# Kernel optimization log

Hardware: AMD Instinct MI355X
Metric: run time of the kernel (lower is better)

The kernel has to match this reference:

```python
import jax, jax.numpy as jnp
import numpy as np

DIM = 256
HEADS = 8
WINDOWS = (1, 2, 4)
B, H, W = 1, 64, 64


def _integral(a):
    # double cumsum over last two dims, then zero-pad one row/col at top/left
    s = jnp.cumsum(jnp.cumsum(a, axis=-2), axis=-1)
    pad = [(0, 0)] * (a.ndim - 2) + [(1, 0), (1, 0)]
    return jnp.pad(s, pad)


def _box(P, ws, Ho, Wo):
    # replicate-pad then box-difference; equivalent to the 2x2 [[1,-1],[-1,1]]
    # kernel conv2d with dilation=ws applied in the torch module.
    tp = ws - 1
    r = tp // 2
    l = tp - r
    pad = [(0, 0)] * (P.ndim - 2) + [(l, r), (l, r)]
    Pp = jnp.pad(P, pad, mode='edge')
    return (Pp[..., ws:ws + Ho, ws:ws + Wo] - Pp[..., ws:ws + Ho, :Wo]
            - Pp[..., :Ho, ws:ws + Wo] + Pp[..., :Ho, :Wo])


def setup_inputs() -> dict:
    key = jax.random.key(0)
    ks = jax.random.split(key, 6)
    x = jax.random.normal(ks[0], (B, DIM, H, W), jnp.float32)
    Wq = jax.random.normal(ks[1], (DIM, DIM), jnp.float32) * 0.05
    Wk = jax.random.normal(ks[2], (DIM, DIM), jnp.float32) * 0.05
    Wv = jax.random.normal(ks[3], (DIM, DIM), jnp.float32) * 0.05
    Wout = jax.random.normal(ks[4], (DIM, DIM * len(WINDOWS)), jnp.float32) * 0.05
    bout = jnp.zeros((DIM,), jnp.float32)
    return {"x": x, "Wq": Wq, "Wk": Wk, "Wv": Wv, "Wout": Wout, "bout": bout}


def reference(x, Wq, Wk, Wv, Wout, bout):
    b, C, Hh, Ww = x.shape
    h = HEADS
    d = C // h
    # 1x1 convs (no bias)
    q = jnp.einsum('bchw,oc->bohw', x, Wq).reshape(b * h, d, Hh, Ww)
    k = jnp.einsum('bchw,oc->bohw', x, Wk).reshape(b * h, d, Hh, Ww)
    v = jnp.einsum('bchw,oc->bohw', x, Wv).reshape(b * h, d, Hh, Ww)
    q = jax.nn.sigmoid(q)
    k = jax.nn.sigmoid(k)
    v = v / jnp.maximum(jnp.linalg.norm(v, axis=1, keepdims=True), 1e-12)

    Ik = _integral(k)                                  # (bh, d, H+1, W+1)
    Ikv = _integral(jnp.einsum('bfhw,bghw->bfghw', k, v))  # (bh, d, d, H+1, W+1)

    outs = []
    for w in WINDOWS:
        ws = Hh // w
        wk = _box(Ik, ws, Hh, Ww)    # (bh, d, H, W)
        wkv = _box(Ikv, ws, Hh, Ww)  # (bh, d, d, H, W)
        attn = jnp.einsum('bdhw,bdfhw->bfhw', q, wkv)
        norm = jnp.einsum('bdhw,bdhw->bhw', q, wk)
        attn = attn / (norm[:, None] + 1e-6)
        outs.append(attn.reshape(b, C, Hh, Ww))
    o = jnp.concatenate(outs, axis=1)  # (b, C*len(WINDOWS), H, W)
    return jnp.einsum('bchw,oc->bohw', o, Wout) + bout[None, :, None, None]
```

## Files before the change

kernel.cpp:

```cpp
#include <hip/hip_runtime.h>
#include <math.h>

#define NPIX 4096
#define CHSZ 3145728
#define NRMSZ 98304

template <int CTRL, int RM>
__device__ __forceinline__ float dpp_add(float x) {
    int xi = __builtin_bit_cast(int, x);
    int sh = __builtin_amdgcn_update_dpp(0, xi, CTRL, RM, 0xf, false);
    return x + __builtin_bit_cast(float, sh);
}

__device__ __forceinline__ float wave_iscan(float x) {
    x = dpp_add<0x111, 0xf>(x);
    x = dpp_add<0x112, 0xf>(x);
    x = dpp_add<0x114, 0xf>(x);
    x = dpp_add<0x118, 0xf>(x);
    x = dpp_add<0x142, 0xa>(x);
    x = dpp_add<0x143, 0xc>(x);
    return x;
}

__device__ __forceinline__ void lds_barrier() {
    asm volatile("s_waitcnt lgkmcnt(0)" ::: "memory");
    __builtin_amdgcn_s_barrier();
    __builtin_amdgcn_sched_barrier(0);
}

__global__ __launch_bounds__(256) void qkv_kernel(
    const float* __restrict__ x, const float* __restrict__ Wq,
    const float* __restrict__ Wk, const float* __restrict__ Wv,
    float* __restrict__ qo, float* __restrict__ ko, float* __restrict__ vo)
{
    const int pt = blockIdx.x * 128;
    const int ot = blockIdx.y * 32;
    const int mat = blockIdx.z;
    const float* __restrict__ W = (mat == 0) ? Wq : ((mat == 1) ? Wk : Wv);
    float* __restrict__ out = (mat == 0) ? qo : ((mat == 1) ? ko : vo);

    __shared__ __align__(16) float Xs[32][132];
    __shared__ __align__(16) float Wt[32][36];

    const int t = threadIdx.x;
    const int pc = t & 31;
    const int oc = t >> 5;
    const int xc = t >> 5;
    const int xp = (t & 31) << 2;
    const int lo = t >> 3;
    const int lg = (t & 7) << 2;

    float4 xf[4];
    float4 wf;
#pragma unroll
    for (int i = 0; i < 4; i++)
        xf[i] = *reinterpret_cast<const float4*>(x + (xc + 8 * i) * NPIX + pt + xp);
    wf = *reinterpret_cast<const float4*>(W + (ot + lo) * 256 + lg);

    float acc[4][4];
#pragma unroll
    for (int j = 0; j < 4; j++)
#pragma unroll
        for (int i = 0; i < 4; i++) acc[j][i] = 0.f;

    for (int kt = 0; kt < 256; kt += 32) {
#pragma unroll
        for (int i = 0; i < 4; i++)
            *reinterpret_cast<float4*>(&Xs[xc + 8 * i][xp]) = xf[i];
        Wt[lg + 0][lo] = wf.x;
        Wt[lg + 1][lo] = wf.y;
        Wt[lg + 2][lo] = wf.z;
        Wt[lg + 3][lo] = wf.w;
        __syncthreads();
        if (kt + 32 < 256) {
#pragma unroll
            for (int i = 0; i < 4; i++)
                xf[i] = *reinterpret_cast<const float4*>(
                    x + (kt + 32 + xc + 8 * i) * NPIX + pt + xp);
            wf = *reinterpret_cast<const float4*>(W + (ot + lo) * 256 + kt + 32 + lg);
        }
#pragma unroll
        for (int kk = 0; kk < 32; kk++) {
            float4 a = *reinterpret_cast<const float4*>(&Xs[kk][pc << 2]);
            float av[4] = {a.x, a.y, a.z, a.w};
            float4 b4 = *reinterpret_cast<const float4*>(&Wt[kk][oc << 2]);
            float bv[4] = {b4.x, b4.y, b4.z, b4.w};
#pragma unroll
            for (int j = 0; j < 4; j++)
#pragma unroll
                for (int i = 0; i < 4; i++)
                    acc[j][i] = fmaf(bv[j], av[i], acc[j][i]);
        }
        __syncthreads();
    }

    if (mat < 2) {
#pragma unroll
        for (int j = 0; j < 4; j++) {
            const int o = ot + (oc << 2) + j;
            float4 r;
            r.x = 1.f / (1.f + __expf(-acc[j][0]));
            r.y = 1.f / (1.f + __expf(-acc[j][1]));
            r.z = 1.f / (1.f + __expf(-acc[j][2]));
            r.w = 1.f / (1.f + __expf(-acc[j][3]));
            *reinterpret_cast<float4*>(out + o * NPIX + pt + (pc << 2)) = r;
        }
    } else {
        float* scratch = &Xs[0][0];
        __syncthreads();
#pragma unroll
        for (int i = 0; i < 4; i++) {
            float ss = 0.f;
#pragma unroll
            for (int j = 0; j < 4; j++) ss += acc[j][i] * acc[j][i];
            scratch[oc * 128 + (pc << 2) + i] = ss;
        }
        __syncthreads();
        float scale[4];
#pragma unroll
        for (int i = 0; i < 4; i++) {
            float tot = 0.f;
#pragma unroll
            for (int g = 0; g < 8; g++) tot += scratch[g * 128 + (pc << 2) + i];
            scale[i] = 1.f / fmaxf(sqrtf(tot), 1e-12f);
        }
#pragma unroll
        for (int j = 0; j < 4; j++) {
            const int o = ot + (oc << 2) + j;
            float4 r;
            r.x = acc[j][0] * scale[0];
            r.y = acc[j][1] * scale[1];
            r.z = acc[j][2] * scale[2];
            r.w = acc[j][3] * scale[3];
            *reinterpret_cast<float4*>(out + o * NPIX + pt + (pc << 2)) = r;
        }
    }
}

template <int PD>
__global__ __launch_bounds__(512) void attn_kernel(
    const float* __restrict__ q, const float* __restrict__ k,
    const float* __restrict__ v, float* __restrict__ num, float* __restrict__ nrm)
{
    const int f = blockIdx.x;
    const int head = blockIdx.y;
    const int dg = blockIdx.z;
    const bool isnorm = (f == 32);

    const float* __restrict__ kh = k + (head * 32 + dg * PD) * NPIX;
    const float* __restrict__ qh = q + (head * 32 + dg * PD) * NPIX;
    const float* __restrict__ vf = v + (head * 32 + (isnorm ? 0 : f)) * NPIX;

    __shared__ __align__(16) float Pt[2][65][68];
    __shared__ float csum[2][8][68];

    const int t = threadIdx.x;
    const int lane = t & 63;
    const int wv = t >> 6;

    for (int i = t; i < 2 * 65 * 68; i += 512) (&Pt[0][0][0])[i] = 0.f;

    float vreg[8], kcur[8];
#pragma unroll
    for (int i = 0; i < 8; i++) {
        const int r = wv * 8 + i;
        vreg[i] = isnorm ? 1.f : vf[r * 64 + lane];
        kcur[i] = kh[r * 64 + lane];
    }

    float acc[3][8];
#pragma unroll
    for (int w = 0; w < 3; w++)
#pragma unroll
        for (int i = 0; i < 8; i++) acc[w][i] = 0.f;

    float pv[8], runcur;
    {
        float run = 0.f;
#pragma unroll
        for (int i = 0; i < 8; i++) {
            float rs = wave_iscan(kcur[i] * vreg[i]);
            pv[i] = run;
            run += rs;
        }
        csum[0][wv][lane] = run;
        runcur = run;
        if (PD > 1) {
#pragma unroll
            for (int i = 0; i < 8; i++)
                kcur[i] = kh[1 * NPIX + (wv * 8 + i) * 64 + lane];
        }
    }
    lds_barrier();

    float pvn[8], runn;
    for (int dd = 0; dd < PD; dd++) {
        const int b = dd & 1;
        float off = 0.f;
#pragma unroll
        for (int w2 = 0; w2 < 7; w2++) if (w2 < wv) off += csum[b][w2][lane];
#pragma unroll
        for (int s = 0; s < 2; s++) {
            float4 r4 = make_float4(pv[4 * s] + off, pv[4 * s + 1] + off,
                                    pv[4 * s + 2] + off, pv[4 * s + 3] + off);
            *reinterpret_cast<float4*>(&Pt[b][lane + 1][wv * 8 + 4 * s]) = r4;
        }
        if (wv == 7) Pt[b][lane + 1][64] = off + runcur;
        float qv[8];
#pragma unroll
        for (int g = 0; g < 2; g++)
#pragma unroll
            for (int j = 0; j < 4; j++)
                qv[g * 4 + j] = qh[dd * NPIX + ((wv + 8 * g) * 4 + j) * 64 + lane];
        if (dd + 1 < PD) {
            float run = 0.f;
#pragma unroll
            for (int i = 0; i < 8; i++) {
                float rs = wave_iscan(kcur[i] * vreg[i]);
                pvn[i] = run;
                run += rs;
            }
            csum[b ^ 1][wv][lane] = run;
            runn = run;
            if (dd + 2 < PD) {
#pragma unroll
                for (int i = 0; i < 8; i++)
                    kcur[i] = kh[(dd + 2) * NPIX + (wv * 8 + i) * 64 + lane];
            }
        }
        lds_barrier();
#pragma unroll
        for (int g = 0; g < 2; g++) {
            const int y0 = (wv + 8 * g) * 4;
#pragma unroll
            for (int w = 0; w < 3; w++) {
                const int hw = 32 >> w;
                const int xlo = max(lane - hw, 0);
                const int xhi = min(lane + hw, 64);
                float c0, c1, c2, c3;
                if (y0 + 3 <= hw) {
                    float4 A4 = *reinterpret_cast<const float4*>(&Pt[b][xhi][y0 + hw]);
                    float4 B4 = *reinterpret_cast<const float4*>(&Pt[b][xlo][y0 + hw]);
                    c0 = A4.x - B4.x; c1 = A4.y - B4.y;
                    c2 = A4.z - B4.z; c3 = A4.w - B4.w;
                } else if (y0 + hw >= 64) {
                    float As = Pt[b][xhi][64];
                    float Bs = Pt[b][xlo][64];
                    float4 C4 = *reinterpret_cast<const float4*>(&Pt[b][xhi][y0 - hw]);
                    float4 E4 = *reinterpret_cast<const float4*>(&Pt[b][xlo][y0 - hw]);
                    const float ab = As - Bs;
                    c0 = ab - (C4.x - E4.x); c1 = ab - (C4.y - E4.y);
                    c2 = ab - (C4.z - E4.z); c3 = ab - (C4.w - E4.w);
                } else {
                    float4 A4 = *reinterpret_cast<const float4*>(&Pt[b][xhi][y0 + hw]);
                    float4 B4 = *reinterpret_cast<const float4*>(&Pt[b][xlo][y0 + hw]);
                    float4 C4 = *reinterpret_cast<const float4*>(&Pt[b][xhi][y0 - hw]);
                    float4 E4 = *reinterpret_cast<const float4*>(&Pt[b][xlo][y0 - hw]);
                    c0 = (A4.x - B4.x) - (C4.x - E4.x);
                    c1 = (A4.y - B4.y) - (C4.y - E4.y);
                    c2 = (A4.z - B4.z) - (C4.z - E4.z);
                    c3 = (A4.w - B4.w) - (C4.w - E4.w);
                }
                acc[w][g * 4 + 0] = fmaf(qv[g * 4 + 0], c0, acc[w][g * 4 + 0]);
                acc[w][g * 4 + 1] = fmaf(qv[g * 4 + 1], c1, acc[w][g * 4 + 1]);
                acc[w][g * 4 + 2] = fmaf(qv[g * 4 + 2], c2, acc[w][g * 4 + 2]);
                acc[w][g * 4 + 3] = fmaf(qv[g * 4 + 3], c3, acc[w][g * 4 + 3]);
            }
        }
        if (dd + 1 < PD) {
#pragma unroll
            for (int i = 0; i < 8; i++) pv[i] = pvn[i];
            runcur = runn;
        }
    }

    float* __restrict__ nout = num + (size_t)dg * CHSZ;
    float* __restrict__ rout = nrm + (size_t)dg * NRMSZ;
#pragma unroll
    for (int w = 0; w < 3; w++) {
#pragma unroll
        for (int g = 0; g < 2; g++) {
#pragma unroll
            for (int j = 0; j < 4; j++) {
                const int px = ((wv + 8 * g) * 4 + j) * 64 + lane;
                const float val = acc[w][g * 4 + j];
                if (isnorm) rout[(w * 8 + head) * NPIX + px] = val;
                else        nout[((w * 8 + head) * 32 + f) * NPIX + px] = val;
            }
        }
    }
}

template <int NS>
__global__ __launch_bounds__(256) void out_kernel(
    const float* __restrict__ num, const float* __restrict__ nrm,
    const float* __restrict__ Wout, float* __restrict__ obuf)
{
    const int pt = blockIdx.x * 64;
    const int ot = blockIdx.y * 64;
    const int kt0 = blockIdx.z * 12;
    __shared__ __align__(16) float As[32][68];
    __shared__ __align__(16) float Wt[32][68];
    const int t = threadIdx.x;
    const int pc = t & 15;
    const int oc = t >> 4;
    const int xc = t >> 4;
    const int xp = (t & 15) << 2;
    const int lo = t & 63;
    const int lc = (t >> 6) << 2;

    float4 nv[NS][2], mv[NS], wf[2];
#pragma unroll
    for (int s = 0; s < NS; s++) {
#pragma unroll
        for (int i = 0; i < 2; i++)
            nv[s][i] = *reinterpret_cast<const float4*>(
                num + (size_t)s * CHSZ + (size_t)(kt0 * 32 + xc + 16 * i) * NPIX + pt + xp);
        mv[s] = *reinterpret_cast<const float4*>(
            nrm + (size_t)s * NRMSZ + kt0 * NPIX + pt + xp);
    }
    wf[0] = *reinterpret_cast<const float4*>(Wout + (ot + lo) * 768 + kt0 * 32 + lc);
    wf[1] = *reinterpret_cast<const float4*>(Wout + (ot + lo) * 768 + kt0 * 32 + lc + 16);

    float acc[4][4];
#pragma unroll
    for (int j = 0; j < 4; j++)
#pragma unroll
        for (int i = 0; i < 4; i++) acc[j][i] = 0.f;

    for (int kt = kt0; kt < kt0 + 12; kt++) {
        float4 ms = mv[0];
#pragma unroll
        for (int s = 1; s < NS; s++) {
            ms.x += mv[s].x; ms.y += mv[s].y; ms.z += mv[s].z; ms.w += mv[s].w;
        }
        float4 rv;
        rv.x = 1.f / (ms.x + 1e-6f); rv.y = 1.f / (ms.y + 1e-6f);
        rv.z = 1.f / (ms.z + 1e-6f); rv.w = 1.f / (ms.w + 1e-6f);
#pragma unroll
        for (int i = 0; i < 2; i++) {
            float4 r = nv[0][i];
#pragma unroll
            for (int s = 1; s < NS; s++) {
                r.x += nv[s][i].x; r.y += nv[s][i].y;
                r.z += nv[s][i].z; r.w += nv[s][i].w;
            }
            r.x *= rv.x; r.y *= rv.y; r.z *= rv.z; r.w *= rv.w;
            *reinterpret_cast<float4*>(&As[xc + 16 * i][xp]) = r;
        }
#pragma unroll
        for (int i = 0; i < 2; i++) {
            Wt[lc + 16 * i + 0][lo] = wf[i].x;
            Wt[lc + 16 * i + 1][lo] = wf[i].y;
            Wt[lc + 16 * i + 2][lo] = wf[i].z;
            Wt[lc + 16 * i + 3][lo] = wf[i].w;
        }
        __syncthreads();
        if (kt + 1 < kt0 + 12) {
#pragma unroll
            for (int s = 0; s < NS; s++) {
#pragma unroll
                for (int i = 0; i < 2; i++)
                    nv[s][i] = *reinterpret_cast<const float4*>(
                        num + (size_t)s * CHSZ +
                        (size_t)((kt + 1) * 32 + xc + 16 * i) * NPIX + pt + xp);
                mv[s] = *reinterpret_cast<const float4*>(
                    nrm + (size_t)s * NRMSZ + (kt + 1) * NPIX + pt + xp);
            }
            wf[0] = *reinterpret_cast<const float4*>(
                Wout + (ot + lo) * 768 + (kt + 1) * 32 + lc);
            wf[1] = *reinterpret_cast<const float4*>(
                Wout + (ot + lo) * 768 + (kt + 1) * 32 + lc + 16);
        }
#pragma unroll
        for (int kk = 0; kk < 32; kk++) {
            float4 a = *reinterpret_cast<const float4*>(&As[kk][pc << 2]);
            float av[4] = {a.x, a.y, a.z, a.w};
            float4 b4 = *reinterpret_cast<const float4*>(&Wt[kk][oc << 2]);
            float bv[4] = {b4.x, b4.y, b4.z, b4.w};
#pragma unroll
            for (int j = 0; j < 4; j++)
#pragma unroll
                for (int i = 0; i < 4; i++)
                    acc[j][i] = fmaf(bv[j], av[i], acc[j][i]);
        }
        __syncthreads();
    }

    float* __restrict__ ob = obuf + (size_t)blockIdx.z * 1048576;
#pragma unroll
    for (int j = 0; j < 4; j++) {
        const int o = ot + (oc << 2) + j;
        float4 r;
        r.x = acc[j][0]; r.y = acc[j][1]; r.z = acc[j][2]; r.w = acc[j][3];
        *reinterpret_cast<float4*>(ob + o * NPIX + pt + (pc << 2)) = r;
    }
}

__global__ __launch_bounds__(256) void kmerge_kernel(
    const float* __restrict__ obuf, const float* __restrict__ bout,
    float* __restrict__ out)
{
    const int i4 = (blockIdx.x * 256 + threadIdx.x) * 4;
    const float bb = bout[i4 >> 12];
    float4 a = *reinterpret_cast<const float4*>(obuf + i4);
    float4 b = *reinterpret_cast<const float4*>(obuf + 1048576 + i4);
    float4 r;
    r.x = a.x + b.x + bb;
    r.y = a.y + b.y + bb;
    r.z = a.z + b.z + bb;
    r.w = a.w + b.w + bb;
    *reinterpret_cast<float4*>(out + i4) = r;
}

extern "C" void kernel_launch(void* const* d_in, const int* in_sizes, int n_in,
                              void* d_out, int out_size, void* d_ws, size_t ws_size,
                              hipStream_t stream)
{
    const float* x    = (const float*)d_in[0];
    const float* Wq   = (const float*)d_in[1];
    const float* Wk   = (const float*)d_in[2];
    const float* Wv   = (const float*)d_in[3];
    const float* Wout = (const float*)d_in[4];
    const float* bout = (const float*)d_in[5];
    float* out = (float*)d_out;

    float* ws = (float*)d_ws;
    float* q   = ws;
    float* k   = ws + 1048576;
    float* v   = ws + 2097152;
    float* num = ws + 3145728;
    float* obuf = ws;
    const size_t fl = ws_size / 4;

    qkv_kernel<<<dim3(32, 8, 3), 256, 0, stream>>>(x, Wq, Wk, Wv, q, k, v);

    if (fl >= 3145728 + (size_t)4 * (CHSZ + NRMSZ)) {
        float* nrm = num + (size_t)4 * CHSZ;
        attn_kernel<8><<<dim3(33, 8, 4), 512, 0, stream>>>(q, k, v, num, nrm);
        out_kernel<4><<<dim3(64, 4, 2), 256, 0, stream>>>(num, nrm, Wout, obuf);
    } else if (fl >= 3145728 + (size_t)2 * (CHSZ + NRMSZ)) {
        float* nrm = num + (size_t)2 * CHSZ;
        attn_kernel<16><<<dim3(33, 8, 2), 512, 0, stream>>>(q, k, v, num, nrm);
        out_kernel<2><<<dim3(64, 4, 2), 256, 0, stream>>>(num, nrm, Wout, obuf);
    } else {
        float* nrm = num + CHSZ;
        attn_kernel<32><<<dim3(33, 8, 1), 512, 0, stream>>>(q, k, v, num, nrm);
        out_kernel<1><<<dim3(64, 4, 2), 256, 0, stream>>>(num, nrm, Wout, obuf);
    }
    kmerge_kernel<<<dim3(1024), 256, 0, stream>>>(obuf, bout, out);
}
```

Measured before the change: 142.5 us.

## Store prefix table row-major and assign threads 4 contiguous x pixels

The integral table in LDS is now stored row-major instead of transposed, with scalar stores per row. Each thread now owns four consecutive x pixels in one row instead of four consecutive y pixels in one column. This allows float4 global loads of q, float4 output stores, and a single uniform box-difference path with edge clamping in place of three branch cases. The cost is scalar strided LDS writes during table construction and possible bank conflicts or misaligned float4 reads at the clamped edge offsets.

```diff
diff --git a/kernel.cpp b/kernel.cpp
--- a/kernel.cpp
+++ b/kernel.cpp
@@ -157,6 +157,8 @@
     const int t = threadIdx.x;
     const int lane = t & 63;
     const int wv = t >> 6;
+    const int ty = t >> 4;
+    const int x4 = (t & 15) << 2;
 
     for (int i = t; i < 2 * 65 * 68; i += 512) (&Pt[0][0][0])[i] = 0.f;
 
@@ -200,18 +202,12 @@
 #pragma unroll
         for (int w2 = 0; w2 < 7; w2++) if (w2 < wv) off += csum[b][w2][lane];
 #pragma unroll
-        for (int s = 0; s < 2; s++) {
-            float4 r4 = make_float4(pv[4 * s] + off, pv[4 * s + 1] + off,
-                                    pv[4 * s + 2] + off, pv[4 * s + 3] + off);
-            *reinterpret_cast<float4*>(&Pt[b][lane + 1][wv * 8 + 4 * s]) = r4;
-        }
-        if (wv == 7) Pt[b][lane + 1][64] = off + runcur;
-        float qv[8];
-#pragma unroll
-        for (int g = 0; g < 2; g++)
-#pragma unroll
-            for (int j = 0; j < 4; j++)
-                qv[g * 4 + j] = qh[dd * NPIX + ((wv + 8 * g) * 4 + j) * 64 + lane];
+        for (int i = 0; i < 8; i++)
+            Pt[b][wv * 8 + i][lane + 1] = pv[i] + off;
+        if (wv == 7) Pt[b][64][lane + 1] = off + runcur;
+        float4 qv4[2];
+        qv4[0] = *reinterpret_cast<const float4*>(qh + dd * NPIX + ty * 64 + x4);
+        qv4[1] = *reinterpret_cast<const float4*>(qh + dd * NPIX + (ty + 32) * 64 + x4);
         if (dd + 1 < PD) {
             float run = 0.f;
 #pragma unroll
@@ -231,40 +227,36 @@
         lds_barrier();
 #pragma unroll
         for (int g = 0; g < 2; g++) {
-            const int y0 = (wv + 8 * g) * 4;
+            const int y = ty + 32 * g;
+            const float qx = (g == 0) ? qv4[0].x : qv4[1].x;
+            const float qy = (g == 0) ? qv4[0].y : qv4[1].y;
+            const float qz = (g == 0) ? qv4[0].z : qv4[1].z;
+            const float qw = (g == 0) ? qv4[0].w : qv4[1].w;
 #pragma unroll
             for (int w = 0; w < 3; w++) {
                 const int hw = 32 >> w;
-                const int xlo = max(lane - hw, 0);
-                const int xhi = min(lane + hw, 64);
-                float c0, c1, c2, c3;
-                if (y0 + 3 <= hw) {
-                    float4 A4 = *reinterpret_cast<const float4*>(&Pt[b][xhi][y0 + hw]);
-                    float4 B4 = *reinterpret_cast<const float4*>(&Pt[b][xlo][y0 + hw]);
-                    c0 = A4.x - B4.x; c1 = A4.y - B4.y;
-                    c2 = A4.z - B4.z; c3 = A4.w - B4.w;
-                } else if (y0 + hw >= 64) {
-                    float As = Pt[b][xhi][64];
-                    float Bs = Pt[b][xlo][64];
-                    float4 C4 = *reinterpret_cast<const float4*>(&Pt[b][xhi][y0 - hw]);
-                    float4 E4 = *reinterpret_cast<const float4*>(&Pt[b][xlo][y0 - hw]);
-                    const float ab = As - Bs;
-                    c0 = ab - (C4.x - E4.x); c1 = ab - (C4.y - E4.y);
-                    c2 = ab - (C4.z - E4.z); c3 = ab - (C4.w - E4.w);
-                } else {
-                    float4 A4 = *reinterpret_cast<const float4*>(&Pt[b][xhi][y0 + hw]);
-                    float4 B4 = *reinterpret_cast<const float4*>(&Pt[b][xlo][y0 + hw]);
-                    float4 C4 = *reinterpret_cast<const float4*>(&Pt[b][xhi][y0 - hw]);
-                    float4 E4 = *reinterpret_cast<const float4*>(&Pt[b][xlo][y0 - hw]);
-                    c0 = (A4.x - B4.x) - (C4.x - E4.x);
-                    c1 = (A4.y - B4.y) - (C4.y - E4.y);
-                    c2 = (A4.z - B4.z) - (C4.z - E4.z);
-                    c3 = (A4.w - B4.w) - (C4.w - E4.w);
+                const int yhi = min(y + hw, 64);
+                const int ylo = max(y - hw, 0);
+                const int xh = x4 + hw;
+                const int xl = x4 - hw;
+                const int xhc = min(xh, 64);
+                const int xlc = max(xl, 0);
+                float4 A4 = *reinterpret_cast<const float4*>(&Pt[b][yhi][xhc]);
+                float4 C4 = *reinterpret_cast<const float4*>(&Pt[b][ylo][xhc]);
+                float4 B4 = *reinterpret_cast<const float4*>(&Pt[b][yhi][xlc]);
+                float4 E4 = *reinterpret_cast<const float4*>(&Pt[b][ylo][xlc]);
+                if (xh >= 64) {
+                    A4.y = A4.x; A4.z = A4.x; A4.w = A4.x;
+                    C4.y = C4.x; C4.z = C4.x; C4.w = C4.x;
                 }
-                acc[w][g * 4 + 0] = fmaf(qv[g * 4 + 0], c0, acc[w][g * 4 + 0]);
-                acc[w][g * 4 + 1] = fmaf(qv[g * 4 + 1], c1, acc[w][g * 4 + 1]);
-                acc[w][g * 4 + 2] = fmaf(qv[g * 4 + 2], c2, acc[w][g * 4 + 2]);
-                acc[w][g * 4 + 3] = fmaf(qv[g * 4 + 3], c3, acc[w][g * 4 + 3]);
+                if (xl < 0) {
+                    B4 = make_float4(0.f, 0.f, 0.f, 0.f);
+                    E4 = B4;
+                }
+                acc[w][g * 4 + 0] = fmaf(qx, (A4.x - B4.x) - (C4.x - E4.x), acc[w][g * 4 + 0]);
+                acc[w][g * 4 + 1] = fmaf(qy, (A4.y - B4.y) - (C4.y - E4.y), acc[w][g * 4 + 1]);
+                acc[w][g * 4 + 2] = fmaf(qz, (A4.z - B4.z) - (C4.z - E4.z), acc[w][g * 4 + 2]);
+                acc[w][g * 4 + 3] = fmaf(qw, (A4.w - B4.w) - (C4.w - E4.w), acc[w][g * 4 + 3]);
             }
         }
         if (dd + 1 < PD) {
@@ -280,13 +272,13 @@
     for (int w = 0; w < 3; w++) {
 #pragma unroll
         for (int g = 0; g < 2; g++) {
-#pragma unroll
-            for (int j = 0; j < 4; j++) {
-                const int px = ((wv + 8 * g) * 4 + j) * 64 + lane;
-                const float val = acc[w][g * 4 + j];
-                if (isnorm) rout[(w * 8 + head) * NPIX + px] = val;
-                else        nout[((w * 8 + head) * 32 + f) * NPIX + px] = val;
-            }
+            const int px = (ty + 32 * g) * 64 + x4;
+            float4 r = make_float4(acc[w][g * 4 + 0], acc[w][g * 4 + 1],
+                                   acc[w][g * 4 + 2], acc[w][g * 4 + 3]);
+            if (isnorm)
+                *reinterpret_cast<float4*>(rout + (w * 8 + head) * NPIX + px) = r;
+            else
+                *reinterpret_cast<float4*>(nout + ((w * 8 + head) * 32 + f) * NPIX + px) = r;
         }
     }
 }
```

New measurement: 179.2 us. +25.8%, slower.
